# Performance work log

Measured on AMD Instinct MI355X. Metric: run time of the kernel, lower is better.

The kernel has to match this reference:

```python
import jax, jax.numpy as jnp
import numpy as np

D_MODEL = 2048
NUM_HEADS = 16
D_FF = 8192
BATCH = 4
SEQ = 2048


def setup_inputs() -> dict:
    key = jax.random.key(0)
    ks = jax.random.split(key, 16)
    s_attn = 1.0 / np.sqrt(D_MODEL)
    s_ff1 = 1.0 / np.sqrt(D_MODEL)
    s_ff2 = 1.0 / np.sqrt(D_FF)
    return {
        "x": jax.random.normal(ks[0], (BATCH, SEQ, D_MODEL), dtype=jnp.float32),
        "Wq": jax.random.normal(ks[1], (D_MODEL, D_MODEL), dtype=jnp.float32) * s_attn,
        "bq": jnp.zeros((D_MODEL,), dtype=jnp.float32),
        "Wk": jax.random.normal(ks[2], (D_MODEL, D_MODEL), dtype=jnp.float32) * s_attn,
        "bk": jnp.zeros((D_MODEL,), dtype=jnp.float32),
        "Wv": jax.random.normal(ks[3], (D_MODEL, D_MODEL), dtype=jnp.float32) * s_attn,
        "bv": jnp.zeros((D_MODEL,), dtype=jnp.float32),
        "Wo": jax.random.normal(ks[4], (D_MODEL, D_MODEL), dtype=jnp.float32) * s_attn,
        "bo": jnp.zeros((D_MODEL,), dtype=jnp.float32),
        "W1": jax.random.normal(ks[5], (D_MODEL, D_FF), dtype=jnp.float32) * s_ff1,
        "b1": jnp.zeros((D_FF,), dtype=jnp.float32),
        "W2": jax.random.normal(ks[6], (D_FF, D_MODEL), dtype=jnp.float32) * s_ff2,
        "b2": jnp.zeros((D_MODEL,), dtype=jnp.float32),
        "ln1_g": jnp.ones((D_MODEL,), dtype=jnp.float32),
        "ln1_b": jnp.zeros((D_MODEL,), dtype=jnp.float32),
        "ln2_g": jnp.ones((D_MODEL,), dtype=jnp.float32),
        "ln2_b": jnp.zeros((D_MODEL,), dtype=jnp.float32),
    }


def _layer_norm(x, g, b, eps=1e-5):
    mu = jnp.mean(x, axis=-1, keepdims=True)
    var = jnp.mean(jnp.square(x - mu), axis=-1, keepdims=True)
    return (x - mu) * jax.lax.rsqrt(var + eps) * g + b


def _attention(h, Wq, bq, Wk, bk, Wv, bv, Wo, bo):
    B, S, D = h.shape
    H = NUM_HEADS
    dk = D // H
    q = (h @ Wq + bq).reshape(B, S, H, dk).transpose(0, 2, 1, 3)  # bhsd
    k = (h @ Wk + bk).reshape(B, S, H, dk).transpose(0, 2, 1, 3)
    v = (h @ Wv + bv).reshape(B, S, H, dk).transpose(0, 2, 1, 3)
    logits = jnp.einsum("bhqd,bhkd->bhqk", q, k) / jnp.sqrt(jnp.float32(dk))
    causal = jnp.triu(jnp.ones((S, S), dtype=bool), k=1)  # True above diagonal
    logits = jnp.where(causal, -jnp.inf, logits)
    attn = jax.nn.softmax(logits, axis=-1)
    out = jnp.einsum("bhqk,bhkd->bhqd", attn, v)
    out = out.transpose(0, 2, 1, 3).reshape(B, S, D)
    return out @ Wo + bo


def reference(x, Wq, bq, Wk, bk, Wv, bv, Wo, bo, W1, b1, W2, b2,
              ln1_g, ln1_b, ln2_g, ln2_b):
    # Pre-LN attention block + residual
    h = _layer_norm(x, ln1_g, ln1_b)
    x = x + _attention(h, Wq, bq, Wk, bk, Wv, bv, Wo, bo)
    # Pre-LN FFN block + residual (GELU activation)
    h = _layer_norm(x, ln2_g, ln2_b)
    ff = jax.nn.gelu(h @ W1 + b1, approximate=False) @ W2 + b2
    return x + ff
```

## Files before the change

kernel.cpp:

```cpp
#include <hip/hip_runtime.h>
#include <hip/hip_bf16.h>

#define D_MODEL 2048
#define NUM_HEADS 16
#define D_FF 8192
#define BATCH 4
#define SEQ 2048
#define DK 128
#define MTOT (BATCH * SEQ)

typedef __attribute__((ext_vector_type(8))) short short8;
typedef __attribute__((ext_vector_type(4))) short short4v;
typedef __attribute__((ext_vector_type(4))) float f32x4;

#define MFMA16(a, b, c) __builtin_amdgcn_mfma_f32_16x16x32_bf16(a, b, c, 0, 0, 0)

#define GLOAD16(gp, lp)                                                        \
  __builtin_amdgcn_global_load_lds(                                            \
      (const __attribute__((address_space(1))) void*)(gp),                     \
      (__attribute__((address_space(3))) void*)(lp), 16, 0, 0)

static __device__ __forceinline__ unsigned short f2bf(float f) {
  return __builtin_bit_cast(unsigned short, __float2bfloat16(f));
}

__global__ __launch_bounds__(256) void transpose_cvt_kernel(
    const float* __restrict__ in, __hip_bfloat16* __restrict__ out, int K, int N) {
  __shared__ float tile[32][33];
  const int n0 = blockIdx.x * 32, k0 = blockIdx.y * 32;
  const int tx = threadIdx.x & 31, ty = threadIdx.x >> 5;
#pragma unroll
  for (int i = 0; i < 4; ++i)
    tile[ty + i * 8][tx] = in[(size_t)(k0 + ty + i * 8) * N + n0 + tx];
  __syncthreads();
#pragma unroll
  for (int i = 0; i < 4; ++i)
    out[(size_t)(n0 + ty + i * 8) * K + k0 + tx] = __float2bfloat16(tile[tx][ty + i * 8]);
}

__global__ __launch_bounds__(256) void layernorm_kernel(
    const float* __restrict__ x, const float* __restrict__ g,
    const float* __restrict__ bta, __hip_bfloat16* __restrict__ out) {
  const int row = blockIdx.x;
  const int tid = threadIdx.x;
  const float* xr = x + (size_t)row * D_MODEL;
  float4 v0 = *(const float4*)(xr + tid * 8);
  float4 v1 = *(const float4*)(xr + tid * 8 + 4);
  float s = v0.x + v0.y + v0.z + v0.w + v1.x + v1.y + v1.z + v1.w;
  float q = v0.x * v0.x + v0.y * v0.y + v0.z * v0.z + v0.w * v0.w +
            v1.x * v1.x + v1.y * v1.y + v1.z * v1.z + v1.w * v1.w;
#pragma unroll
  for (int off = 1; off < 64; off <<= 1) {
    s += __shfl_xor(s, off);
    q += __shfl_xor(q, off);
  }
  __shared__ float rs[4], rq[4];
  if ((tid & 63) == 0) {
    rs[tid >> 6] = s;
    rq[tid >> 6] = q;
  }
  __syncthreads();
  s = rs[0] + rs[1] + rs[2] + rs[3];
  q = rq[0] + rq[1] + rq[2] + rq[3];
  const float mu = s * (1.0f / D_MODEL);
  const float var = q * (1.0f / D_MODEL) - mu * mu;
  const float rstd = rsqrtf(var + 1e-5f);
  float4 g0 = *(const float4*)(g + tid * 8);
  float4 g1 = *(const float4*)(g + tid * 8 + 4);
  float4 b0 = *(const float4*)(bta + tid * 8);
  float4 b1 = *(const float4*)(bta + tid * 8 + 4);
  short8 o;
  o[0] = (short)f2bf((v0.x - mu) * rstd * g0.x + b0.x);
  o[1] = (short)f2bf((v0.y - mu) * rstd * g0.y + b0.y);
  o[2] = (short)f2bf((v0.z - mu) * rstd * g0.z + b0.z);
  o[3] = (short)f2bf((v0.w - mu) * rstd * g0.w + b0.w);
  o[4] = (short)f2bf((v1.x - mu) * rstd * g1.x + b1.x);
  o[5] = (short)f2bf((v1.y - mu) * rstd * g1.y + b1.y);
  o[6] = (short)f2bf((v1.z - mu) * rstd * g1.z + b1.z);
  o[7] = (short)f2bf((v1.w - mu) * rstd * g1.w + b1.w);
  *(short8*)(out + (size_t)row * D_MODEL + tid * 8) = o;
}

enum { EPI_BF16 = 0, EPI_VT = 1, EPI_RESID = 2, EPI_GELU = 3 };

template <int EPI>
__global__ __launch_bounds__(256, 2) void gemm_kernel(
    const __hip_bfloat16* __restrict__ A, const __hip_bfloat16* __restrict__ Bt,
    const float* __restrict__ bias, const float* __restrict__ resid,
    void* __restrict__ outv, int M, int N, int K) {
  __shared__ __align__(16) unsigned char sA[16384];
  __shared__ __align__(16) unsigned char sB[16384];
  const int tid = threadIdx.x;
  const int lane = tid & 63, w = tid >> 6;
  const int l15 = lane & 15, lg = lane >> 4;
  const int m0 = blockIdx.y * 128, n0 = blockIdx.x * 128;
  const int wm = (w >> 1) * 64, wn = (w & 1) * 64;

  f32x4 acc[4][4] = {};

  const int row8 = lane >> 3;
  const int g8 = (lane & 7) ^ row8;

  for (int kt = 0; kt < K; kt += 64) {
#pragma unroll
    for (int i = 0; i < 4; ++i) {
      const int c = w * 4 + i;
      const int row = c * 8 + row8;
      GLOAD16(A + (size_t)(m0 + row) * K + kt + g8 * 8, sA + c * 1024);
      GLOAD16(Bt + (size_t)(n0 + row) * K + kt + g8 * 8, sB + c * 1024);
    }
    __syncthreads();
#pragma unroll
    for (int ks = 0; ks < 2; ++ks) {
      const int cb = ks * 4 + lg;
      short8 af[4], bf[4];
#pragma unroll
      for (int f = 0; f < 4; ++f) {
        const int ra = wm + f * 16 + l15;
        af[f] = *(const short8*)(sA + ra * 128 + ((cb ^ (ra & 7)) << 4));
        const int rb = wn + f * 16 + l15;
        bf[f] = *(const short8*)(sB + rb * 128 + ((cb ^ (rb & 7)) << 4));
      }
#pragma unroll
      for (int fi = 0; fi < 4; ++fi)
#pragma unroll
        for (int fj = 0; fj < 4; ++fj)
          acc[fi][fj] = MFMA16(af[fi], bf[fj], acc[fi][fj]);
    }
    __syncthreads();
  }

#pragma unroll
  for (int fi = 0; fi < 4; ++fi) {
#pragma unroll
    for (int fj = 0; fj < 4; ++fj) {
      const int mb = m0 + wm + fi * 16 + lg * 4;
      const int n = n0 + wn + fj * 16 + l15;
      const float bv = bias ? bias[n] : 0.0f;
      if constexpr (EPI == EPI_VT) {
        const int bb = mb >> 11, ss = mb & (SEQ - 1);
        const int hh = n >> 7, dd = n & (DK - 1);
        short4v pk;
#pragma unroll
        for (int r = 0; r < 4; ++r) pk[r] = (short)f2bf(acc[fi][fj][r] + bv);
        __hip_bfloat16* o = (__hip_bfloat16*)outv;
        *(short4v*)(o + ((size_t)((bb * NUM_HEADS + hh) * DK + dd)) * SEQ + ss) = pk;
      } else {
#pragma unroll
        for (int r = 0; r < 4; ++r) {
          const int m = mb + r;
          const float v = acc[fi][fj][r] + bv;
          if constexpr (EPI == EPI_BF16) {
            ((__hip_bfloat16*)outv)[(size_t)m * N + n] = __float2bfloat16(v);
          } else if constexpr (EPI == EPI_GELU) {
            const float ge = 0.5f * v * (1.0f + erff(v * 0.70710678118654752f));
            ((__hip_bfloat16*)outv)[(size_t)m * N + n] = __float2bfloat16(ge);
          } else {
            ((float*)outv)[(size_t)m * N + n] = resid[(size_t)m * N + n] + v;
          }
        }
      }
    }
  }
}

__global__ __launch_bounds__(512, 4) void attn_kernel(
    const __hip_bfloat16* __restrict__ Qm, const __hip_bfloat16* __restrict__ Km,
    const __hip_bfloat16* __restrict__ Vt, __hip_bfloat16* __restrict__ Om) {
  __shared__ __align__(16) unsigned char Kl[16384];
  __shared__ __align__(16) unsigned char Vl[16384];
  __shared__ __align__(16) unsigned char Pl[32768];
  const int tid = threadIdx.x;
  const int lane = tid & 63, w = tid >> 6;
  const int l15 = lane & 15, lg = lane >> 4;
  const int bh = blockIdx.y, b = bh >> 4, h = bh & 15;
  const int q0 = blockIdx.x * 128;
  const int qw = q0 + w * 16;
  const int row8 = lane >> 3;

  short8 qf[4];
  const __hip_bfloat16* qbase = Qm + (size_t)(b * SEQ + qw + l15) * D_MODEL + h * DK;
#pragma unroll
  for (int ks = 0; ks < 4; ++ks) qf[ks] = *(const short8*)(qbase + ks * 32 + lg * 8);

  float m_run[4], l_run[4];
  f32x4 acc_o[8];
#pragma unroll
  for (int r = 0; r < 4; ++r) { m_run[r] = -1e30f; l_run[r] = 0.0f; }
#pragma unroll
  for (int fd = 0; fd < 8; ++fd) acc_o[fd] = (f32x4){0.f, 0.f, 0.f, 0.f};

  for (int t0 = 0; t0 < q0 + 128; t0 += 64) {
#pragma unroll
    for (int i = 0; i < 2; ++i) {
      const int c = w * 2 + i;
      const int row = c * 4 + lg;
      const int gcb = l15 ^ (row & 7);
      GLOAD16(Km + (size_t)(b * SEQ + t0 + row) * D_MODEL + h * DK + gcb * 8,
              Kl + c * 1024);
    }
#pragma unroll
    for (int i = 0; i < 2; ++i) {
      const int c = w * 2 + i;
      const int row = c * 8 + row8;
      const int gcb = (lane & 7) ^ (row & 7);
      GLOAD16(Vt + (size_t)(bh * DK + row) * SEQ + t0 + gcb * 8, Vl + c * 1024);
    }
    __syncthreads();
    if (t0 <= qw + 15) {
      f32x4 sacc[4];
#pragma unroll
      for (int fn = 0; fn < 4; ++fn) sacc[fn] = (f32x4){0.f, 0.f, 0.f, 0.f};
#pragma unroll
      for (int ks = 0; ks < 4; ++ks) {
        const int cb = ks * 4 + lg;
#pragma unroll
        for (int fn = 0; fn < 4; ++fn) {
          const int rn = fn * 16 + l15;
          short8 kf = *(const short8*)(Kl + rn * 256 + ((cb ^ (rn & 7)) << 4));
          sacc[fn] = MFMA16(qf[ks], kf, sacc[fn]);
        }
      }
      const float scale = 0.088388347648318447f;
      float mt[4] = {-1e30f, -1e30f, -1e30f, -1e30f};
#pragma unroll
      for (int fn = 0; fn < 4; ++fn) {
        const int key = t0 + fn * 16 + l15;
#pragma unroll
        for (int r = 0; r < 4; ++r) {
          const int qg = qw + lg * 4 + r;
          float sv = sacc[fn][r] * scale;
          sv = (key <= qg) ? sv : -1e30f;
          sacc[fn][r] = sv;
          mt[r] = fmaxf(mt[r], sv);
        }
      }
      float alpha[4], ls[4];
#pragma unroll
      for (int r = 0; r < 4; ++r) {
#pragma unroll
        for (int off = 1; off < 16; off <<= 1) mt[r] = fmaxf(mt[r], __shfl_xor(mt[r], off));
        const float mnew = fmaxf(m_run[r], mt[r]);
        alpha[r] = __expf(m_run[r] - mnew);
        m_run[r] = mnew;
        ls[r] = 0.0f;
      }
#pragma unroll
      for (int fn = 0; fn < 4; ++fn)
#pragma unroll
        for (int r = 0; r < 4; ++r) {
          const float p = __expf(sacc[fn][r] - m_run[r]);
          sacc[fn][r] = p;
          ls[r] += p;
        }
#pragma unroll
      for (int r = 0; r < 4; ++r) {
#pragma unroll
        for (int off = 1; off < 16; off <<= 1) ls[r] += __shfl_xor(ls[r], off);
        l_run[r] = l_run[r] * alpha[r] + ls[r];
      }
#pragma unroll
      for (int fd = 0; fd < 8; ++fd)
#pragma unroll
        for (int r = 0; r < 4; ++r) acc_o[fd][r] *= alpha[r];
      unsigned char* pw = Pl + w * 4096;
#pragma unroll
      for (int fn = 0; fn < 4; ++fn) {
        const int t = fn * 16 + l15;
#pragma unroll
        for (int r = 0; r < 4; ++r) {
          const int qq = lg * 4 + r;
          *(float*)(pw + qq * 256 + (((t >> 3) ^ (qq & 7)) << 5) + (t & 7) * 4) =
              sacc[fn][r];
        }
      }
#pragma unroll
      for (int ks = 0; ks < 2; ++ks) {
        const int cb = ks * 4 + lg;
        const int qq = l15;
        const float4* pp =
            (const float4*)(pw + qq * 256 + ((cb ^ (qq & 7)) << 5));
        const float4 pa = pp[0], pb = pp[1];
        short8 pf;
        pf[0] = (short)f2bf(pa.x); pf[1] = (short)f2bf(pa.y);
        pf[2] = (short)f2bf(pa.z); pf[3] = (short)f2bf(pa.w);
        pf[4] = (short)f2bf(pb.x); pf[5] = (short)f2bf(pb.y);
        pf[6] = (short)f2bf(pb.z); pf[7] = (short)f2bf(pb.w);
#pragma unroll
        for (int fd = 0; fd < 8; ++fd) {
          const int rv = fd * 16 + l15;
          short8 vf = *(const short8*)(Vl + rv * 128 + ((cb ^ (rv & 7)) << 4));
          acc_o[fd] = MFMA16(pf, vf, acc_o[fd]);
        }
      }
    }
    __syncthreads();
  }
#pragma unroll
  for (int r = 0; r < 4; ++r) {
    const float inv = 1.0f / l_run[r];
    const int qg = qw + lg * 4 + r;
    __hip_bfloat16* ob = Om + (size_t)(b * SEQ + qg) * D_MODEL + h * DK + l15;
#pragma unroll
    for (int fd = 0; fd < 8; ++fd)
      ob[fd * 16] = __float2bfloat16(acc_o[fd][r] * inv);
  }
}

extern "C" void kernel_launch(void* const* d_in, const int* in_sizes, int n_in,
                              void* d_out, int out_size, void* d_ws, size_t ws_size,
                              hipStream_t stream) {
  (void)in_sizes; (void)n_in; (void)out_size;
  const size_t MB = 1024 * 1024;
  if (ws_size < 192 * MB) return;

  const float* x  = (const float*)d_in[0];
  const float* Wq = (const float*)d_in[1];
  const float* bq = (const float*)d_in[2];
  const float* Wk = (const float*)d_in[3];
  const float* bk = (const float*)d_in[4];
  const float* Wv = (const float*)d_in[5];
  const float* bv = (const float*)d_in[6];
  const float* Wo = (const float*)d_in[7];
  const float* bo = (const float*)d_in[8];
  const float* W1 = (const float*)d_in[9];
  const float* b1 = (const float*)d_in[10];
  const float* W2 = (const float*)d_in[11];
  const float* b2 = (const float*)d_in[12];
  const float* g1 = (const float*)d_in[13];
  const float* be1 = (const float*)d_in[14];
  const float* g2 = (const float*)d_in[15];
  const float* be2 = (const float*)d_in[16];

  char* ws = (char*)d_ws;
  __hip_bfloat16* Hb  = (__hip_bfloat16*)(ws + 0 * MB);
  __hip_bfloat16* Qb  = (__hip_bfloat16*)(ws + 32 * MB);
  __hip_bfloat16* Kb  = (__hip_bfloat16*)(ws + 64 * MB);
  __hip_bfloat16* Vtb = (__hip_bfloat16*)(ws + 96 * MB);
  __hip_bfloat16* AOb = (__hip_bfloat16*)(ws + 128 * MB);
  __hip_bfloat16* W1T = (__hip_bfloat16*)(ws + 32 * MB);
  __hip_bfloat16* W2T = (__hip_bfloat16*)(ws + 64 * MB);
  __hip_bfloat16* FF1 = (__hip_bfloat16*)(ws + 96 * MB);
  __hip_bfloat16* WqT = (__hip_bfloat16*)(ws + 160 * MB);
  __hip_bfloat16* WkT = (__hip_bfloat16*)(ws + 168 * MB);
  __hip_bfloat16* WvT = (__hip_bfloat16*)(ws + 176 * MB);
  __hip_bfloat16* WoT = (__hip_bfloat16*)(ws + 184 * MB);
  float* X2 = (float*)d_out;

  const dim3 tb(256);
  transpose_cvt_kernel<<<dim3(64, 64), tb, 0, stream>>>(Wq, WqT, 2048, 2048);
  transpose_cvt_kernel<<<dim3(64, 64), tb, 0, stream>>>(Wk, WkT, 2048, 2048);
  transpose_cvt_kernel<<<dim3(64, 64), tb, 0, stream>>>(Wv, WvT, 2048, 2048);
  transpose_cvt_kernel<<<dim3(64, 64), tb, 0, stream>>>(Wo, WoT, 2048, 2048);

  layernorm_kernel<<<MTOT, tb, 0, stream>>>(x, g1, be1, Hb);

  const dim3 gQKV(2048 / 128, MTOT / 128);
  gemm_kernel<EPI_BF16><<<gQKV, tb, 0, stream>>>(Hb, WqT, bq, nullptr, Qb, MTOT, 2048, 2048);
  gemm_kernel<EPI_BF16><<<gQKV, tb, 0, stream>>>(Hb, WkT, bk, nullptr, Kb, MTOT, 2048, 2048);
  gemm_kernel<EPI_VT><<<gQKV, tb, 0, stream>>>(Hb, WvT, bv, nullptr, Vtb, MTOT, 2048, 2048);

  attn_kernel<<<dim3(SEQ / 128, BATCH * NUM_HEADS), dim3(512), 0, stream>>>(Qb, Kb, Vtb, AOb);

  transpose_cvt_kernel<<<dim3(256, 64), tb, 0, stream>>>(W1, W1T, 2048, 8192);
  transpose_cvt_kernel<<<dim3(64, 256), tb, 0, stream>>>(W2, W2T, 8192, 2048);

  gemm_kernel<EPI_RESID><<<gQKV, tb, 0, stream>>>(AOb, WoT, bo, x, X2, MTOT, 2048, 2048);

  layernorm_kernel<<<MTOT, tb, 0, stream>>>(X2, g2, be2, Hb);

  for (int c = 0; c < 2; ++c) {
    const size_t moff = (size_t)c * 4096;
    gemm_kernel<EPI_GELU><<<dim3(8192 / 128, 4096 / 128), tb, 0, stream>>>(
        Hb + moff * D_MODEL, W1T, b1, nullptr, FF1, 4096, 8192, 2048);
    gemm_kernel<EPI_RESID><<<dim3(2048 / 128, 4096 / 128), tb, 0, stream>>>(
        FF1, W2T, b2, X2 + moff * D_MODEL, X2 + moff * D_MODEL, 4096, 2048, 8192);
  }
}
```

Measured before the change: 1.434 ms.

## Rewrite GEMM as 256x256-tile, 512-thread kernel with 4-stage LDS pipeline

The GEMM kernel now uses 512 threads, 256x256 output tiles with K-step 32, and a 4-deep ring of LDS buffers filled by async global-to-LDS loads. Explicit vmcnt waits replace the load/sync/compute/sync pattern, so loads overlap MFMA work. A 1D grid with XCD-aware block swizzling improves L2 locality. The cost is much higher register pressure from 32 accumulators per thread and 128KB of LDS per block, which limits occupancy. The W2 GEMM grid shrinks to 128 blocks, which may underfill the GPU.

```diff
diff --git a/kernel.cpp b/kernel.cpp
--- a/kernel.cpp
+++ b/kernel.cpp
@@ -84,54 +84,74 @@
 enum { EPI_BF16 = 0, EPI_VT = 1, EPI_RESID = 2, EPI_GELU = 3 };
 
 template <int EPI>
-__global__ __launch_bounds__(256, 2) void gemm_kernel(
+__global__ __launch_bounds__(512, 2) void gemm_kernel(
     const __hip_bfloat16* __restrict__ A, const __hip_bfloat16* __restrict__ Bt,
     const float* __restrict__ bias, const float* __restrict__ resid,
-    void* __restrict__ outv, int M, int N, int K) {
-  __shared__ __align__(16) unsigned char sA[16384];
-  __shared__ __align__(16) unsigned char sB[16384];
+    void* __restrict__ outv, int M, int N, int K, int nby) {
+  __shared__ __align__(16) unsigned char lds[4][32768];
   const int tid = threadIdx.x;
   const int lane = tid & 63, w = tid >> 6;
   const int l15 = lane & 15, lg = lane >> 4;
-  const int m0 = blockIdx.y * 128, n0 = blockIdx.x * 128;
-  const int wm = (w >> 1) * 64, wn = (w & 1) * 64;
-
-  f32x4 acc[4][4] = {};
-
-  const int row8 = lane >> 3;
-  const int g8 = (lane & 7) ^ row8;
-
-  for (int kt = 0; kt < K; kt += 64) {
-#pragma unroll
-    for (int i = 0; i < 4; ++i) {
-      const int c = w * 4 + i;
-      const int row = c * 8 + row8;
-      GLOAD16(A + (size_t)(m0 + row) * K + kt + g8 * 8, sA + c * 1024);
-      GLOAD16(Bt + (size_t)(n0 + row) * K + kt + g8 * 8, sB + c * 1024);
-    }
-    __syncthreads();
-#pragma unroll
-    for (int ks = 0; ks < 2; ++ks) {
-      const int cb = ks * 4 + lg;
-      short8 af[4], bf[4];
-#pragma unroll
-      for (int f = 0; f < 4; ++f) {
-        const int ra = wm + f * 16 + l15;
-        af[f] = *(const short8*)(sA + ra * 128 + ((cb ^ (ra & 7)) << 4));
-        const int rb = wn + f * 16 + l15;
-        bf[f] = *(const short8*)(sB + rb * 128 + ((cb ^ (rb & 7)) << 4));
-      }
-#pragma unroll
-      for (int fi = 0; fi < 4; ++fi)
-#pragma unroll
-        for (int fj = 0; fj < 4; ++fj)
-          acc[fi][fj] = MFMA16(af[fi], bf[fj], acc[fi][fj]);
-    }
-    __syncthreads();
-  }
-
-#pragma unroll
-  for (int fi = 0; fi < 4; ++fi) {
+  const int bid = blockIdx.x;
+  const int cpx = gridDim.x >> 3;
+  const int swz = (bid & 7) * cpx + (bid >> 3);
+  const int m0 = (swz % nby) * 256, n0 = (swz / nby) * 256;
+  const int wm = (w >> 2) * 128, wn = (w & 3) * 64;
+
+  const int rsub = lane >> 2;
+  const int gblk = (lane & 3) ^ ((lane >> 2) & 3) ^ ((lane >> 4) & 3);
+  const int off16 = (lg ^ ((l15 & 3) ^ ((l15 >> 2) & 3))) << 4;
+
+  const int cA = w * 2;
+  const __hip_bfloat16* Asrc = A + (size_t)(m0 + cA * 16 + rsub) * K + gblk * 8;
+  const __hip_bfloat16* Bsrc = Bt + (size_t)(n0 + cA * 16 + rsub) * K + gblk * 8;
+  const size_t rstep = (size_t)16 * K;
+
+  f32x4 acc[8][4] = {};
+  const int nt = K >> 5;
+
+  auto STAGE = [&](int tt) {
+    unsigned char* db = lds[tt & 3];
+    const size_t ko = (size_t)tt * 32;
+    GLOAD16(Asrc + ko, db + cA * 1024);
+    GLOAD16(Asrc + rstep + ko, db + cA * 1024 + 1024);
+    GLOAD16(Bsrc + ko, db + 16384 + cA * 1024);
+    GLOAD16(Bsrc + rstep + ko, db + 16384 + cA * 1024 + 1024);
+  };
+  auto COMPUTE = [&](int tt) {
+    const unsigned char* db = lds[tt & 3];
+    short8 af[8], bfr[4];
+#pragma unroll
+    for (int fj = 0; fj < 4; ++fj)
+      bfr[fj] = *(const short8*)(db + 16384 + (wn + fj * 16 + l15) * 64 + off16);
+#pragma unroll
+    for (int fi = 0; fi < 8; ++fi)
+      af[fi] = *(const short8*)(db + (wm + fi * 16 + l15) * 64 + off16);
+#pragma unroll
+    for (int fi = 0; fi < 8; ++fi)
+#pragma unroll
+      for (int fj = 0; fj < 4; ++fj)
+        acc[fi][fj] = MFMA16(af[fi], bfr[fj], acc[fi][fj]);
+  };
+
+  STAGE(0);
+  STAGE(1);
+  STAGE(2);
+  for (int t = 0; t < nt - 2; ++t) {
+    asm volatile("s_waitcnt vmcnt(8)" ::: "memory");
+    __builtin_amdgcn_s_barrier();
+    if (t + 3 < nt) STAGE(t + 3);
+    COMPUTE(t);
+  }
+  asm volatile("s_waitcnt vmcnt(4)" ::: "memory");
+  __builtin_amdgcn_s_barrier();
+  COMPUTE(nt - 2);
+  asm volatile("s_waitcnt vmcnt(0)" ::: "memory");
+  __builtin_amdgcn_s_barrier();
+  COMPUTE(nt - 1);
+
+#pragma unroll
+  for (int fi = 0; fi < 8; ++fi) {
 #pragma unroll
     for (int fj = 0; fj < 4; ++fj) {
       const int mb = m0 + wm + fi * 16 + lg * 4;
@@ -355,25 +375,24 @@
 
   layernorm_kernel<<<MTOT, tb, 0, stream>>>(x, g1, be1, Hb);
 
-  const dim3 gQKV(2048 / 128, MTOT / 128);
-  gemm_kernel<EPI_BF16><<<gQKV, tb, 0, stream>>>(Hb, WqT, bq, nullptr, Qb, MTOT, 2048, 2048);
-  gemm_kernel<EPI_BF16><<<gQKV, tb, 0, stream>>>(Hb, WkT, bk, nullptr, Kb, MTOT, 2048, 2048);
-  gemm_kernel<EPI_VT><<<gQKV, tb, 0, stream>>>(Hb, WvT, bv, nullptr, Vtb, MTOT, 2048, 2048);
+  gemm_kernel<EPI_BF16><<<256, 512, 0, stream>>>(Hb, WqT, bq, nullptr, Qb, MTOT, 2048, 2048, 32);
+  gemm_kernel<EPI_BF16><<<256, 512, 0, stream>>>(Hb, WkT, bk, nullptr, Kb, MTOT, 2048, 2048, 32);
+  gemm_kernel<EPI_VT><<<256, 512, 0, stream>>>(Hb, WvT, bv, nullptr, Vtb, MTOT, 2048, 2048, 32);
 
   attn_kernel<<<dim3(SEQ / 128, BATCH * NUM_HEADS), dim3(512), 0, stream>>>(Qb, Kb, Vtb, AOb);
 
   transpose_cvt_kernel<<<dim3(256, 64), tb, 0, stream>>>(W1, W1T, 2048, 8192);
   transpose_cvt_kernel<<<dim3(64, 256), tb, 0, stream>>>(W2, W2T, 8192, 2048);
 
-  gemm_kernel<EPI_RESID><<<gQKV, tb, 0, stream>>>(AOb, WoT, bo, x, X2, MTOT, 2048, 2048);
+  gemm_kernel<EPI_RESID><<<256, 512, 0, stream>>>(AOb, WoT, bo, x, X2, MTOT, 2048, 2048, 32);
 
   layernorm_kernel<<<MTOT, tb, 0, stream>>>(X2, g2, be2, Hb);
 
   for (int c = 0; c < 2; ++c) {
     const size_t moff = (size_t)c * 4096;
-    gemm_kernel<EPI_GELU><<<dim3(8192 / 128, 4096 / 128), tb, 0, stream>>>(
-        Hb + moff * D_MODEL, W1T, b1, nullptr, FF1, 4096, 8192, 2048);
-    gemm_kernel<EPI_RESID><<<dim3(2048 / 128, 4096 / 128), tb, 0, stream>>>(
-        FF1, W2T, b2, X2 + moff * D_MODEL, X2 + moff * D_MODEL, 4096, 2048, 8192);
-  }
-}
+    gemm_kernel<EPI_GELU><<<512, 512, 0, stream>>>(
+        Hb + moff * D_MODEL, W1T, b1, nullptr, FF1, 4096, 8192, 2048, 16);
+    gemm_kernel<EPI_RESID><<<128, 512, 0, stream>>>(
+        FF1, W2T, b2, X2 + moff * D_MODEL, X2 + moff * D_MODEL, 4096, 2048, 8192, 16);
+  }
+}
```

Result: slower. 1.520 ms (+6.0%).

## Double-buffer K/V tiles in attention and store P as bf16 in LDS

Applied to the files above, without the earlier changes.

The attention kernel now prefetches the next K/V tile into a second LDS buffer while computing on the current one, using vmcnt waits and raw barriers instead of full syncthreads. The softmax probabilities are converted to bf16 before being written to LDS, which halves the P buffer and removes the per-read conversion. This aims to hide global load latency and cut LDS traffic, but it raises total LDS use and may affect occupancy. A leftover no-op loop remains in the code.

```diff
diff --git a/kernel.cpp b/kernel.cpp
--- a/kernel.cpp
+++ b/kernel.cpp
@@ -167,9 +167,9 @@
 __global__ __launch_bounds__(512, 4) void attn_kernel(
     const __hip_bfloat16* __restrict__ Qm, const __hip_bfloat16* __restrict__ Km,
     const __hip_bfloat16* __restrict__ Vt, __hip_bfloat16* __restrict__ Om) {
-  __shared__ __align__(16) unsigned char Kl[16384];
-  __shared__ __align__(16) unsigned char Vl[16384];
-  __shared__ __align__(16) unsigned char Pl[32768];
+  __shared__ __align__(16) unsigned char Kl[2][16384];
+  __shared__ __align__(16) unsigned char Vl[2][16384];
+  __shared__ __align__(16) unsigned char Pl[16384];
   const int tid = threadIdx.x;
   const int lane = tid & 63, w = tid >> 6;
   const int l15 = lane & 15, lg = lane >> 4;
@@ -177,6 +177,7 @@
   const int q0 = blockIdx.x * 128;
   const int qw = q0 + w * 16;
   const int row8 = lane >> 3;
+  const int nt = (q0 >> 6) + 2;
 
   short8 qf[4];
   const __hip_bfloat16* qbase = Qm + (size_t)(b * SEQ + qw + l15) * D_MODEL + h * DK;
@@ -190,24 +191,41 @@
 #pragma unroll
   for (int fd = 0; fd < 8; ++fd) acc_o[fd] = (f32x4){0.f, 0.f, 0.f, 0.f};
 
-  for (int t0 = 0; t0 < q0 + 128; t0 += 64) {
+  auto STAGE = [&](int tt) {
+    unsigned char* kb = Kl[tt & 1];
+    unsigned char* vb = Vl[tt & 1];
+    const int t0 = tt * 64;
 #pragma unroll
     for (int i = 0; i < 2; ++i) {
       const int c = w * 2 + i;
       const int row = c * 4 + lg;
       const int gcb = l15 ^ (row & 7);
       GLOAD16(Km + (size_t)(b * SEQ + t0 + row) * D_MODEL + h * DK + gcb * 8,
-              Kl + c * 1024);
+              kb + c * 1024);
     }
 #pragma unroll
     for (int i = 0; i < 2; ++i) {
       const int c = w * 2 + i;
       const int row = c * 8 + row8;
       const int gcb = (lane & 7) ^ (row & 7);
-      GLOAD16(Vt + (size_t)(bh * DK + row) * SEQ + t0 + gcb * 8, Vl + c * 1024);
-    }
-    __syncthreads();
+      GLOAD16(Vt + (size_t)(bh * DK + row) * SEQ + t0 + gcb * 8, vb + c * 1024);
+    }
+  };
+
+  STAGE(0);
+  for (int t = 0; t < nt; ++t) {
+    const int t0 = t * 64;
+    if (t + 1 < nt) {
+      STAGE(t + 1);
+      asm volatile("s_waitcnt vmcnt(4)" ::: "memory");
+    } else {
+      asm volatile("s_waitcnt vmcnt(0)" ::: "memory");
+    }
+    __builtin_amdgcn_s_barrier();
+    asm volatile("" ::: "memory");
     if (t0 <= qw + 15) {
+      const unsigned char* kb = Kl[t & 1];
+      const unsigned char* vb = Vl[t & 1];
       f32x4 sacc[4];
 #pragma unroll
       for (int fn = 0; fn < 4; ++fn) sacc[fn] = (f32x4){0.f, 0.f, 0.f, 0.f};
@@ -217,7 +235,7 @@
 #pragma unroll
         for (int fn = 0; fn < 4; ++fn) {
           const int rn = fn * 16 + l15;
-          short8 kf = *(const short8*)(Kl + rn * 256 + ((cb ^ (rn & 7)) << 4));
+          short8 kf = *(const short8*)(kb + rn * 256 + ((cb ^ (rn & 7)) << 4));
           sacc[fn] = MFMA16(qf[ks], kf, sacc[fn]);
         }
       }
@@ -263,38 +281,38 @@
       for (int fd = 0; fd < 8; ++fd)
 #pragma unroll
         for (int r = 0; r < 4; ++r) acc_o[fd][r] *= alpha[r];
-      unsigned char* pw = Pl + w * 4096;
+      unsigned char* pw = Pl + w * 2048;
 #pragma unroll
       for (int fn = 0; fn < 4; ++fn) {
-        const int t = fn * 16 + l15;
+        const int tt = fn * 16 + l15;
 #pragma unroll
         for (int r = 0; r < 4; ++r) {
           const int qq = lg * 4 + r;
-          *(float*)(pw + qq * 256 + (((t >> 3) ^ (qq & 7)) << 5) + (t & 7) * 4) =
-              sacc[fn][r];
+          *(unsigned short*)(pw + qq * 128 + (((tt >> 3) ^ (qq & 7)) << 4) +
+                             (tt & 7) * 2) = f2bf(sacc[fn][r]);
         }
       }
 #pragma unroll
       for (int ks = 0; ks < 2; ++ks) {
+#pragma unroll
+        for (int half = 0; half < 2; ++half) {
+          const int tb = (ks * 2 + half) * 2 + (lg & 1) + (lg >> 1) * 0;
+        }
+        const int tb = ks * 4 + lg;
+        short8 pf = *(const short8*)(Pl + w * 2048 + l15 * 128 +
+                                     ((tb ^ (l15 & 7)) << 4));
         const int cb = ks * 4 + lg;
-        const int qq = l15;
-        const float4* pp =
-            (const float4*)(pw + qq * 256 + ((cb ^ (qq & 7)) << 5));
-        const float4 pa = pp[0], pb = pp[1];
-        short8 pf;
-        pf[0] = (short)f2bf(pa.x); pf[1] = (short)f2bf(pa.y);
-        pf[2] = (short)f2bf(pa.z); pf[3] = (short)f2bf(pa.w);
-        pf[4] = (short)f2bf(pb.x); pf[5] = (short)f2bf(pb.y);
-        pf[6] = (short)f2bf(pb.z); pf[7] = (short)f2bf(pb.w);
 #pragma unroll
         for (int fd = 0; fd < 8; ++fd) {
           const int rv = fd * 16 + l15;
-          short8 vf = *(const short8*)(Vl + rv * 128 + ((cb ^ (rv & 7)) << 4));
+          short8 vf = *(const short8*)(vb + rv * 128 + ((cb ^ (rv & 7)) << 4));
           acc_o[fd] = MFMA16(pf, vf, acc_o[fd]);
         }
       }
     }
-    __syncthreads();
+    asm volatile("" ::: "memory");
+    __builtin_amdgcn_s_barrier();
+    asm volatile("" ::: "memory");
   }
 #pragma unroll
   for (int r = 0; r < 4; ++r) {
```

After: 1.376 ms. -4.1%, faster.
